# Performance work log

Measured on AMD Instinct MI355X. Metric: run time of the kernel, lower is better.

## Reference

```python
import jax, jax.numpy as jnp
import numpy as np
from jax import lax

C = 256
HEADS = 8
H2 = HEADS // 2          # heads per branch
HD = C // HEADS          # head dim = 32
SR = 4                   # spatial reduction ratio
WS = 7                   # window size (hard-coded in source)
SCALE = HD ** -0.5
EPS = 1e-5


def _window_partition(t, H, W, D):
    # t: [B, h, N, c] -> [B*h*nW, WS^3, c]
    B, h, N, c = t.shape
    t = t.reshape(B * h, H // WS, WS, W // WS, WS, D // WS, WS, c)
    t = t.transpose(0, 1, 3, 5, 2, 4, 6, 7)
    return t.reshape(-1, WS * WS * WS, c)


def _window_reverse(w, H, W, D, head):
    # w: [BH*nW, WS^3, c] -> [B, N, head*c] (heads interleaved into channels)
    nW = (H // WS) * (W // WS) * (D // WS)
    BH = w.shape[0] // nW
    x = w.reshape(BH, H // WS, W // WS, D // WS, WS, WS, WS, -1)
    x = x.transpose(0, 1, 4, 2, 5, 3, 6, 7).reshape(BH, H, W, D, -1)
    B = BH // head
    x = x.reshape(B, head, H, W, D, -1).transpose(0, 2, 3, 4, 1, 5)
    return x.reshape(B, H * W * D, -1)


def setup_inputs() -> dict:
    key = jax.random.key(0)
    ks = jax.random.split(key, 16)
    B, H, W, D = 1, 28, 28, 28
    N = H * W * D
    tn = lambda k, shp: jax.random.normal(k, shp, jnp.float32) * 0.02
    # conv fan-out inits (per source _init_weights)
    lepe_fan = 3 * 3 * C // C  # depthwise: groups=C
    sr_fan = SR * SR * C
    return {
        "x": jax.random.normal(ks[0], (B, N, C), jnp.float32),
        "H": H, "W": W, "D": D,
        "lepe_w": tn(ks[1], (C, C)),
        "lepe_b": jnp.zeros((C,), jnp.float32),
        "lepe_conv_w": jax.random.normal(ks[2], (C, 1, 3, 3, 3), jnp.float32) * np.sqrt(2.0 / lepe_fan),
        "lepe_conv_b": jnp.zeros((C,), jnp.float32),
        "sr_w": jax.random.normal(ks[3], (C, C, SR, SR, SR), jnp.float32) * np.sqrt(2.0 / sr_fan),
        "sr_b": jnp.zeros((C,), jnp.float32),
        "norm_g": jnp.ones((C,), jnp.float32),
        "norm_b": jnp.zeros((C,), jnp.float32),
        "q1_w": tn(ks[4], (C // 2, C)),
        "kv1_w": tn(ks[5], (C, C)),
        "q2_w": tn(ks[6], (C // 2, C)),
        "kv2_w": tn(ks[7], (C, C)),
        "proj_w": tn(ks[8], (C, C)),
        "proj_b": jnp.zeros((C,), jnp.float32),
    }


def _forward(x, lepe_w, lepe_b, lepe_conv_w, lepe_conv_b, sr_w, sr_b,
             norm_g, norm_b, q1_w, kv1_w, q2_w, kv2_w, proj_w, proj_b,
             H, W, D):
    B, N, _ = x.shape
    # --- LePE: linear -> depthwise Conv3d over (H,W,D) ---
    y = x @ lepe_w.T + lepe_b                              # [B,N,C]
    y = y.transpose(0, 2, 1).reshape(B, C, H, W, D)
    lepe = lax.conv_general_dilated(
        y, lepe_conv_w, window_strides=(1, 1, 1), padding='SAME',
        dimension_numbers=('NCDHW', 'OIDHW', 'NCDHW'), feature_group_count=C)
    lepe = (lepe + lepe_conv_b[None, :, None, None, None])
    lepe = lepe.reshape(B, C, N).transpose(0, 2, 1)        # [B,N,C]

    x_ = x.transpose(0, 2, 1).reshape(B, C, H, W, D)

    # --- Branch 1: spatially-reduced global attention (heads 0..3) ---
    q1 = (x @ q1_w.T).reshape(B, N, H2, HD).transpose(0, 2, 1, 3)   # [B,h2,N,hd]
    x1 = lax.conv_general_dilated(
        x_, sr_w, window_strides=(SR, SR, SR), padding='VALID',
        dimension_numbers=('NCDHW', 'OIDHW', 'NCDHW'))
    x1 = x1 + sr_b[None, :, None, None, None]
    x1 = x1.reshape(B, C, -1).transpose(0, 2, 1)                    # [B,Nr,C]
    mu = x1.mean(-1, keepdims=True)
    var = ((x1 - mu) ** 2).mean(-1, keepdims=True)
    x1 = (x1 - mu) * lax.rsqrt(var + EPS) * norm_g + norm_b
    x1 = jax.nn.gelu(x1, approximate=False)
    Nr = x1.shape[1]
    kv1 = (x1 @ kv1_w.T).reshape(B, Nr, 2, H2, HD).transpose(2, 0, 3, 1, 4)
    k1, v1 = kv1[0], kv1[1]                                         # [B,h2,Nr,hd]
    attn1 = jax.nn.softmax(jnp.einsum('bhnd,bhmd->bhnm', q1, k1) * SCALE, axis=-1)
    o1 = jnp.einsum('bhnm,bhmd->bhnd', attn1, v1)
    o1 = o1.transpose(0, 2, 1, 3).reshape(B, N, C // 2)

    # --- Branch 2: windowed local attention (heads 4..7) ---
    q2 = (x @ q2_w.T).reshape(B, N, H2, HD).transpose(0, 2, 1, 3)
    kv2 = (x @ kv2_w.T).reshape(B, N, 2, H2, HD).transpose(2, 0, 3, 1, 4)
    k2, v2 = kv2[0], kv2[1]                                         # [B,h2,N,hd]
    q2w = _window_partition(q2, H, W, D)
    k2w = _window_partition(k2, H, W, D)
    v2w = _window_partition(v2, H, W, D)
    attn2 = jax.nn.softmax(jnp.einsum('wnd,wmd->wnm', q2w, k2w) * SCALE, axis=-1)
    o2 = jnp.einsum('wnm,wmd->wnd', attn2, v2w)
    o2 = _window_reverse(o2, H, W, D, H2)                           # [B,N,C/2]

    out = jnp.concatenate([o1, o2], axis=-1)
    return (out + lepe) @ proj_w.T + proj_b


def reference(x, H, W, D, lepe_w, lepe_b, lepe_conv_w, lepe_conv_b,
              sr_w, sr_b, norm_g, norm_b, q1_w, kv1_w, q2_w, kv2_w,
              proj_w, proj_b):
    return _forward(x, lepe_w, lepe_b, lepe_conv_w, lepe_conv_b, sr_w, sr_b,
                    norm_g, norm_b, q1_w, kv1_w, q2_w, kv2_w, proj_w, proj_b,
                    int(H), int(W), int(D))
```

## Files before the change

kernel.cpp:

```cpp
#include <hip/hip_runtime.h>

#define N_TOK 21952
#define NR    343
#define ATT_SCALE 0.17677669529663687f

typedef unsigned short u16;
typedef short  v8s __attribute__((ext_vector_type(8)));
typedef float  v4f __attribute__((ext_vector_type(4)));

__device__ __forceinline__ float bf2f(unsigned u) {
    return __builtin_bit_cast(float, u << 16);
}
__device__ __forceinline__ u16 f2bf(float f) {
    unsigned u = __builtin_bit_cast(unsigned, f);
    u += 0x7fffu + ((u >> 16) & 1u);
    return (u16)(u >> 16);
}
__device__ __forceinline__ unsigned bfadd2(unsigned a, unsigned b) {
    float lo = bf2f(a & 0xffffu) + bf2f(b & 0xffffu);
    float hi = bf2f(a >> 16)     + bf2f(b >> 16);
    return (unsigned)f2bf(lo) | ((unsigned)f2bf(hi) << 16);
}

__global__ __launch_bounds__(256) void convert_x_kernel(
    const float* __restrict__ x, u16* __restrict__ xb)
{
    size_t i = ((size_t)blockIdx.x * 256 + threadIdx.x) * 8;
    float4 a0 = *(const float4*)(x + i);
    float4 a1 = *(const float4*)(x + i + 4);
    uint4 av;
    av.x = (unsigned)f2bf(a0.x) | ((unsigned)f2bf(a0.y) << 16);
    av.y = (unsigned)f2bf(a0.z) | ((unsigned)f2bf(a0.w) << 16);
    av.z = (unsigned)f2bf(a1.x) | ((unsigned)f2bf(a1.y) << 16);
    av.w = (unsigned)f2bf(a1.z) | ((unsigned)f2bf(a1.w) << 16);
    *(uint4*)(xb + i) = av;
}

#define WSEG0 16384
#define WSEG1 24576
#define WSEG2 32768
#define WSEG3 49152
#define WSEG4 65536
#define WSEG5 81920
#define WSEG6 82112

__global__ __launch_bounds__(256) void convert_w_kernel(
    const float* __restrict__ wl,  const float* __restrict__ wq1,
    const float* __restrict__ wq2, const float* __restrict__ wk2,
    const float* __restrict__ wk1, const float* __restrict__ wp,
    const float* __restrict__ lepe_b,
    u16* wb_comb, u16* wb_k1, u16* wb_p, float* bias_all)
{
    int gid = blockIdx.x * 256 + threadIdx.x;
    if (gid >= WSEG6) return;
    if (gid >= WSEG5) {
        int b = gid - WSEG5;
        float4 v;
        int i = b * 4;
        v.x = (i + 0 < 256) ? lepe_b[i + 0] : 0.f;
        v.y = (i + 1 < 256) ? lepe_b[i + 1] : 0.f;
        v.z = (i + 2 < 256) ? lepe_b[i + 2] : 0.f;
        v.w = (i + 3 < 256) ? lepe_b[i + 3] : 0.f;
        *(float4*)(bias_all + i) = v;
        return;
    }
    const float* s; u16* d; int l; float sc = 1.f;
    if      (gid < WSEG0) { s = wl;  d = wb_comb;           l = gid; }
    else if (gid < WSEG1) { s = wq1; d = wb_comb + 65536;   l = gid - WSEG0; sc = ATT_SCALE; }
    else if (gid < WSEG2) { s = wq2; d = wb_comb + 98304;   l = gid - WSEG1; sc = ATT_SCALE; }
    else if (gid < WSEG3) { s = wk2; d = wb_comb + 131072;  l = gid - WSEG2; }
    else if (gid < WSEG4) { s = wk1; d = wb_k1;             l = gid - WSEG3; }
    else                  { s = wp;  d = wb_p;              l = gid - WSEG4; }
    float4 v = *(const float4*)(s + (size_t)l * 4);
    *(ushort4*)(d + (size_t)l * 4) =
        make_ushort4(f2bf(v.x * sc), f2bf(v.y * sc), f2bf(v.z * sc), f2bf(v.w * sc));
}

__global__ __launch_bounds__(256) void convert_sr_kernel(
    const float* __restrict__ wsr, u16* __restrict__ wt)
{
    int u  = blockIdx.x * 256 + threadIdx.x;
    int co = u >> 8, ci = u & 255;
    const float* src = wsr + (size_t)co * 16384 + ci * 64;
#pragma unroll
    for (int t4 = 0; t4 < 16; t4++) {
        float4 v = *(const float4*)(src + t4 * 4);
        int t = t4 * 4;
        wt[(size_t)(t + 0) * 65536 + co * 256 + ci] = f2bf(v.x);
        wt[(size_t)(t + 1) * 65536 + co * 256 + ci] = f2bf(v.y);
        wt[(size_t)(t + 2) * 65536 + co * 256 + ci] = f2bf(v.z);
        wt[(size_t)(t + 3) * 65536 + co * 256 + ci] = f2bf(v.w);
    }
}

#define LDK 136

__global__ __launch_bounds__(256, 3) void gemm_k256(
    const u16* __restrict__ A, const u16* __restrict__ A2,
    const u16* __restrict__ W, const float* __restrict__ bias,
    void* __restrict__ outp, int M, int ldout, int mode, int nwg, int NT)
{
    __shared__ u16 Asm[128 * LDK];
    __shared__ u16 Bsm[64 * LDK];
    const int tid = threadIdx.x;

    int bid = blockIdx.x;
    int q = nwg >> 3, r = nwg & 7;
    int xcd = bid & 7, idx = bid >> 3;
    int wgid = (xcd < r ? xcd * (q + 1) : r * (q + 1) + (xcd - r) * q) + idx;
    const int m0 = (wgid / NT) * 128;
    const int n0 = (wgid % NT) * 64;

    const int wave = tid >> 6, lane = tid & 63;
    const int wm = (wave & 1) * 64, wn = (wave >> 1) * 32;
    const int fr = lane & 15, fq = lane >> 4;

    v4f acc[4][2];
#pragma unroll
    for (int i = 0; i < 4; i++)
#pragma unroll
        for (int j = 0; j < 2; j++) acc[i][j] = (v4f){0.f, 0.f, 0.f, 0.f};

    for (int ph = 0; ph < 2; ph++) {
        const int kb = ph * 128;
#pragma unroll
        for (int i = 0; i < 8; i++) {
            int u = tid + i * 256;
            int rr = u >> 4, seg = (u & 15) * 8;
            uint4 av = make_uint4(0, 0, 0, 0);
            int m = m0 + rr;
            if (m < M) {
                av = *(const uint4*)(A + (size_t)m * 256 + kb + seg);
                if (A2) {
                    uint4 bv = *(const uint4*)(A2 + (size_t)m * 256 + kb + seg);
                    av.x = bfadd2(av.x, bv.x); av.y = bfadd2(av.y, bv.y);
                    av.z = bfadd2(av.z, bv.z); av.w = bfadd2(av.w, bv.w);
                }
            }
            *(uint4*)(Asm + rr * LDK + seg) = av;
        }
#pragma unroll
        for (int i = 0; i < 4; i++) {
            int u = tid + i * 256;
            int rr = u >> 4, seg = (u & 15) * 8;
            uint4 wv = *(const uint4*)(W + (size_t)(n0 + rr) * 256 + kb + seg);
            *(uint4*)(Bsm + rr * LDK + seg) = wv;
        }
        __syncthreads();

#pragma unroll
        for (int kk = 0; kk < 128; kk += 32) {
            v8s af[4], bf[2];
#pragma unroll
            for (int i = 0; i < 4; i++)
                af[i] = *(const v8s*)(Asm + (wm + i * 16 + fr) * LDK + kk + fq * 8);
#pragma unroll
            for (int j = 0; j < 2; j++)
                bf[j] = *(const v8s*)(Bsm + (wn + j * 16 + fr) * LDK + kk + fq * 8);
#pragma unroll
            for (int i = 0; i < 4; i++)
#pragma unroll
                for (int j = 0; j < 2; j++)
                    acc[i][j] = __builtin_amdgcn_mfma_f32_16x16x32_bf16(
                        af[i], bf[j], acc[i][j], 0, 0, 0);
        }
        __syncthreads();
    }

    float* outf = (float*)outp;
    u16*   outb = (u16*)outp;
#pragma unroll
    for (int i = 0; i < 4; i++) {
#pragma unroll
        for (int j = 0; j < 2; j++) {
            int col = n0 + wn + j * 16 + fr;
#pragma unroll
            for (int rr = 0; rr < 4; rr++) {
                int row = m0 + wm + i * 16 + fq * 4 + rr;
                if (row >= M) continue;
                float v = acc[i][j][rr];
                if (bias) v += bias[col];
                if (mode == 0) outb[(size_t)row * ldout + col] = f2bf(v);
                else           outf[(size_t)row * ldout + col] = v;
            }
        }
    }
}

#define LDA 40

__global__ __launch_bounds__(256) void sr_gemm(
    const u16* __restrict__ xb, const u16* __restrict__ Wt,
    float* __restrict__ partials)
{
    __shared__ u16 Asm[128 * LDA];
    __shared__ u16 Bsm[64 * LDA];
    const int tid = threadIdx.x;
    const int m0 = blockIdx.x * 128;
    const int n0 = blockIdx.y * 64;
    const int z  = blockIdx.z;
    const int wave = tid >> 6, lane = tid & 63;
    const int wm = (wave & 1) * 64, wn = (wave >> 1) * 32;
    const int fr = lane & 15, fq = lane >> 4;

    v4f acc[4][2];
#pragma unroll
    for (int i = 0; i < 4; i++)
#pragma unroll
        for (int j = 0; j < 2; j++) acc[i][j] = (v4f){0.f, 0.f, 0.f, 0.f};

    for (int it = 0; it < 16; it++) {
        int tap = z * 2 + (it >> 3);
        int ci0 = (it & 7) * 32;
        int kz = tap >> 4, ky = (tap >> 2) & 3, kx = tap & 3;
#pragma unroll
        for (int i = 0; i < 2; i++) {
            int u = tid + i * 256;
            int r = u >> 2, seg = (u & 3) * 8;
            uint4 av = make_uint4(0, 0, 0, 0);
            int p = m0 + r;
            if (p < NR) {
                int pz = p / 49, pr = p % 49, py = pr / 7, px = pr % 7;
                int n = (pz * 4 + kz) * 784 + (py * 4 + ky) * 28 + (px * 4 + kx);
                av = *(const uint4*)(xb + (size_t)n * 256 + ci0 + seg);
            }
            *(uint4*)(Asm + r * LDA + seg) = av;
        }
        {
            int r = tid >> 2, seg = (tid & 3) * 8;
            uint4 wv = *(const uint4*)(Wt + (size_t)tap * 65536 +
                                       (size_t)(n0 + r) * 256 + ci0 + seg);
            *(uint4*)(Bsm + r * LDA + seg) = wv;
        }
        __syncthreads();

        v8s af[4], bfr[2];
#pragma unroll
        for (int i = 0; i < 4; i++)
            af[i] = *(const v8s*)(Asm + (wm + i * 16 + fr) * LDA + fq * 8);
#pragma unroll
        for (int j = 0; j < 2; j++)
            bfr[j] = *(const v8s*)(Bsm + (wn + j * 16 + fr) * LDA + fq * 8);
#pragma unroll
        for (int i = 0; i < 4; i++)
#pragma unroll
            for (int j = 0; j < 2; j++)
                acc[i][j] = __builtin_amdgcn_mfma_f32_16x16x32_bf16(
                    af[i], bfr[j], acc[i][j], 0, 0, 0);
        __syncthreads();
    }

    float* dst = partials + (size_t)z * (NR * 256);
#pragma unroll
    for (int i = 0; i < 4; i++) {
#pragma unroll
        for (int j = 0; j < 2; j++) {
            int col = n0 + wn + j * 16 + fr;
#pragma unroll
            for (int r = 0; r < 4; r++) {
                int row = m0 + wm + i * 16 + fq * 4 + r;
                if (row < NR) dst[(size_t)row * 256 + col] = acc[i][j][r];
            }
        }
    }
}

__global__ __launch_bounds__(256) void ln_gelu_kernel(
    const float* __restrict__ partials, const float* __restrict__ srb,
    const float* __restrict__ g, const float* __restrict__ b,
    u16* __restrict__ out)
{
    int row = blockIdx.x, c = threadIdx.x;
    float v = srb[c];
#pragma unroll
    for (int s = 0; s < 32; s++)
        v += partials[(size_t)s * (NR * 256) + row * 256 + c];
    float s1 = v, s2 = v * v;
#pragma unroll
    for (int off = 1; off < 64; off <<= 1) {
        s1 += __shfl_xor(s1, off);
        s2 += __shfl_xor(s2, off);
    }
    __shared__ float ws[4], ws2[4];
    int wave = c >> 6, lane = c & 63;
    if (lane == 0) { ws[wave] = s1; ws2[wave] = s2; }
    __syncthreads();
    float mean = (ws[0] + ws[1] + ws[2] + ws[3]) * (1.f / 256.f);
    float m2   = (ws2[0] + ws2[1] + ws2[2] + ws2[3]) * (1.f / 256.f);
    float var  = m2 - mean * mean;
    float xn = (v - mean) * rsqrtf(var + 1e-5f) * g[c] + b[c];
    out[row * 256 + c] = f2bf(0.5f * xn * (1.f + erff(xn * 0.70710678118654752f)));
}

__global__ __launch_bounds__(256) void dwconv_kernel(
    const u16* __restrict__ xall, const float* __restrict__ w,
    const float* __restrict__ bias, u16* __restrict__ out)
{
    __shared__ float sm[216 * 64];
    __shared__ float sw[64 * 27];
    const int tid = threadIdx.x;
    const int t  = blockIdx.x;
    const int g  = blockIdx.y;
    const int tz = t / 49, tr = t % 49, ty = tr / 7, tx = tr % 7;

    for (int u = tid; u < 64 * 27; u += 256) sw[u] = w[g * 64 * 27 + u];

    for (int u = tid; u < 216 * 8; u += 256) {
        int r = u >> 3, c8 = (u & 7) * 8;
        int vz = tz * 4 - 1 + r / 36;
        int rem = r % 36;
        int vy = ty * 4 - 1 + rem / 6;
        int vx = tx * 4 - 1 + rem % 6;
        float f[8];
        if ((unsigned)vz < 28u && (unsigned)vy < 28u && (unsigned)vx < 28u) {
            int n = vz * 784 + vy * 28 + vx;
            uint4 raw = *(const uint4*)(xall + (size_t)n * 768 + g * 64 + c8);
            f[0] = bf2f(raw.x & 0xffffu); f[1] = bf2f(raw.x >> 16);
            f[2] = bf2f(raw.y & 0xffffu); f[3] = bf2f(raw.y >> 16);
            f[4] = bf2f(raw.z & 0xffffu); f[5] = bf2f(raw.z >> 16);
            f[6] = bf2f(raw.w & 0xffffu); f[7] = bf2f(raw.w >> 16);
        } else {
#pragma unroll
            for (int i = 0; i < 8; i++) f[i] = 0.f;
        }
        float* dst = &sm[r * 64 + c8];
        *(float4*)dst       = make_float4(f[0], f[1], f[2], f[3]);
        *(float4*)(dst + 4) = make_float4(f[4], f[5], f[6], f[7]);
    }
    __syncthreads();

    const int c  = tid & 63;
    const int ch = g * 64 + c;
    float wreg[27];
#pragma unroll
    for (int j = 0; j < 27; j++) wreg[j] = sw[c * 27 + j];
    const float bc = bias[ch];

    const int vbase = (tid >> 6) * 16;
    for (int v = vbase; v < vbase + 16; v++) {
        int vz = v >> 4, vy = (v >> 2) & 3, vx = v & 3;
        float a = bc;
#pragma unroll
        for (int dz = 0; dz < 3; dz++)
#pragma unroll
            for (int dy = 0; dy < 3; dy++)
#pragma unroll
                for (int dx = 0; dx < 3; dx++)
                    a = fmaf(sm[((vz + dz) * 36 + (vy + dy) * 6 + (vx + dx)) * 64 + c],
                             wreg[dz * 9 + dy * 3 + dx], a);
        int n = (tz * 4 + vz) * 784 + (ty * 4 + vy) * 28 + (tx * 4 + vx);
        out[(size_t)n * 256 + ch] = f2bf(a);
    }
}

#define KP  40
#define VTP 360
#define PP  40

__global__ __launch_bounds__(256) void attn1_kernel(
    const u16* __restrict__ xall, const u16* __restrict__ kv1,
    u16* __restrict__ o)
{
    __shared__ u16 Ks[352 * KP];
    __shared__ u16 VTs[32 * VTP];
    __shared__ u16 Ps[4 * 16 * PP];
    const int tid = threadIdx.x;
    const int h = blockIdx.y;
    const int qbase = blockIdx.x * 352;
    const int mt0 = blockIdx.z * 11;
    const int wave = tid >> 6, lane = tid & 63;
    const int fr = lane & 15, fq = lane >> 4;

    for (int u = tid; u < 352 * 4; u += 256) {
        int r = u >> 2, seg = u & 3;
        uint4 kq = make_uint4(0, 0, 0, 0), vq = make_uint4(0, 0, 0, 0);
        if (r < NR) {
            kq = *(const uint4*)(kv1 + (size_t)r * 256 + h * 32 + seg * 8);
            vq = *(const uint4*)(kv1 + (size_t)r * 256 + 128 + h * 32 + seg * 8);
        }
        *(uint4*)(Ks + r * KP + seg * 8) = kq;
        int d0 = seg * 8;
        VTs[(d0 + 0) * VTP + r] = (u16)(vq.x & 0xffffu);
        VTs[(d0 + 1) * VTP + r] = (u16)(vq.x >> 16);
        VTs[(d0 + 2) * VTP + r] = (u16)(vq.y & 0xffffu);
        VTs[(d0 + 3) * VTP + r] = (u16)(vq.y >> 16);
        VTs[(d0 + 4) * VTP + r] = (u16)(vq.z & 0xffffu);
        VTs[(d0 + 5) * VTP + r] = (u16)(vq.z >> 16);
        VTs[(d0 + 6) * VTP + r] = (u16)(vq.w & 0xffffu);
        VTs[(d0 + 7) * VTP + r] = (u16)(vq.w >> 16);
    }
    __syncthreads();

    u16* Pw = Ps + wave * 16 * PP;
    for (int mt = mt0 + wave; mt < mt0 + 11; mt += 4) {
        int qrow = qbase + mt * 16 + fr;
        v8s aq = {0, 0, 0, 0, 0, 0, 0, 0};
        if (qrow < N_TOK)
            aq = *(const v8s*)(xall + (size_t)qrow * 768 + 256 + h * 32 + fq * 8);

        v4f s[22];
#pragma unroll
        for (int t = 0; t < 22; t++) {
            v8s bk = *(const v8s*)(Ks + (t * 16 + fr) * KP + fq * 8);
            s[t] = __builtin_amdgcn_mfma_f32_16x16x32_bf16(
                aq, bk, (v4f){0.f, 0.f, 0.f, 0.f}, 0, 0, 0);
        }
        if (fr >= 7) {
#pragma unroll
            for (int r = 0; r < 4; r++) s[21][r] = -1e30f;
        }

        float inv_l[4];
#pragma unroll
        for (int r = 0; r < 4; r++) {
            float m = s[0][r];
#pragma unroll
            for (int t = 1; t < 22; t++) m = fmaxf(m, s[t][r]);
#pragma unroll
            for (int off = 1; off < 16; off <<= 1) m = fmaxf(m, __shfl_xor(m, off));
            float l = 0.f;
#pragma unroll
            for (int t = 0; t < 22; t++) {
                v4f sv = s[t];
                float p = __expf(sv[r] - m);
                sv[r] = p; s[t] = sv;
                l += p;
            }
#pragma unroll
            for (int off = 1; off < 16; off <<= 1) l += __shfl_xor(l, off);
            inv_l[r] = 1.f / l;
        }

        v4f o0 = {0.f, 0.f, 0.f, 0.f}, o1 = {0.f, 0.f, 0.f, 0.f};
#pragma unroll
        for (int kt = 0; kt < 11; kt++) {
#pragma unroll
            for (int tt = 0; tt < 2; tt++) {
                int t = kt * 2 + tt;
#pragma unroll
                for (int r = 0; r < 4; r++)
                    Pw[(fq * 4 + r) * PP + tt * 16 + fr] = f2bf(s[t][r]);
            }
            __asm__ volatile("s_waitcnt lgkmcnt(0)" ::: "memory");
            v8s ap  = *(const v8s*)(Pw + fr * PP + fq * 8);
            v8s bv0 = *(const v8s*)(VTs + fr * VTP + kt * 32 + fq * 8);
            v8s bv1 = *(const v8s*)(VTs + (16 + fr) * VTP + kt * 32 + fq * 8);
            o0 = __builtin_amdgcn_mfma_f32_16x16x32_bf16(ap, bv0, o0, 0, 0, 0);
            o1 = __builtin_amdgcn_mfma_f32_16x16x32_bf16(ap, bv1, o1, 0, 0, 0);
        }

#pragma unroll
        for (int r = 0; r < 4; r++) {
            int n = qbase + mt * 16 + fq * 4 + r;
            if (n < N_TOK) {
                u16* op = o + (size_t)n * 256 + h * 32;
                op[fr]      = f2bf(o0[r] * inv_l[r]);
                op[16 + fr] = f2bf(o1[r] * inv_l[r]);
            }
        }
    }
}

__global__ __launch_bounds__(256) void attn2_kernel(
    const u16* __restrict__ xall, u16* __restrict__ o)
{
    __shared__ u16 Ks[352 * KP];
    __shared__ u16 VTs[32 * VTP];
    __shared__ u16 Ps[4 * 16 * PP];
    const int tid = threadIdx.x;
    const int h  = blockIdx.y;
    const int wi = blockIdx.x;
    const int zb = (wi >> 4) & 3, yb = (wi >> 2) & 3, xb = wi & 3;
    const int mt0 = blockIdx.z * 11;
    const int wave = tid >> 6, lane = tid & 63;
    const int fr = lane & 15, fq = lane >> 4;

    for (int u = tid; u < 352 * 4; u += 256) {
        int r = u >> 2, seg = u & 3;
        uint4 kq = make_uint4(0, 0, 0, 0), vq = make_uint4(0, 0, 0, 0);
        if (r < NR) {
            int mz = r / 49, mr = r % 49, my = mr / 7, mx = mr % 7;
            int nk = (zb * 7 + mz) * 784 + (yb * 7 + my) * 28 + (xb * 7 + mx);
            const u16* base = xall + (size_t)nk * 768 + 512;
            kq = *(const uint4*)(base + h * 32 + seg * 8);
            vq = *(const uint4*)(base + 128 + h * 32 + seg * 8);
        }
        *(uint4*)(Ks + r * KP + seg * 8) = kq;
        int d0 = seg * 8;
        VTs[(d0 + 0) * VTP + r] = (u16)(vq.x & 0xffffu);
        VTs[(d0 + 1) * VTP + r] = (u16)(vq.x >> 16);
        VTs[(d0 + 2) * VTP + r] = (u16)(vq.y & 0xffffu);
        VTs[(d0 + 3) * VTP + r] = (u16)(vq.y >> 16);
        VTs[(d0 + 4) * VTP + r] = (u16)(vq.z & 0xffffu);
        VTs[(d0 + 5) * VTP + r] = (u16)(vq.z >> 16);
        VTs[(d0 + 6) * VTP + r] = (u16)(vq.w & 0xffffu);
        VTs[(d0 + 7) * VTP + r] = (u16)(vq.w >> 16);
    }
    __syncthreads();

    u16* Pw = Ps + wave * 16 * PP;
    for (int mt = mt0 + wave; mt < mt0 + 11; mt += 4) {
        int tw = mt * 16 + fr;
        v8s aq = {0, 0, 0, 0, 0, 0, 0, 0};
        if (tw < NR) {
            int wz = tw / 49, tr2 = tw % 49, wy = tr2 / 7, wx = tr2 % 7;
            int nq = (zb * 7 + wz) * 784 + (yb * 7 + wy) * 28 + (xb * 7 + wx);
            aq = *(const v8s*)(xall + (size_t)nq * 768 + 384 + h * 32 + fq * 8);
        }

        v4f s[22];
#pragma unroll
        for (int t = 0; t < 22; t++) {
            v8s bk = *(const v8s*)(Ks + (t * 16 + fr) * KP + fq * 8);
            s[t] = __builtin_amdgcn_mfma_f32_16x16x32_bf16(
                aq, bk, (v4f){0.f, 0.f, 0.f, 0.f}, 0, 0, 0);
        }
        if (fr >= 7) {
#pragma unroll
            for (int r = 0; r < 4; r++) s[21][r] = -1e30f;
        }

        float inv_l[4];
#pragma unroll
        for (int r = 0; r < 4; r++) {
            float m = s[0][r];
#pragma unroll
            for (int t = 1; t < 22; t++) m = fmaxf(m, s[t][r]);
#pragma unroll
            for (int off = 1; off < 16; off <<= 1) m = fmaxf(m, __shfl_xor(m, off));
            float l = 0.f;
#pragma unroll
            for (int t = 0; t < 22; t++) {
                v4f sv = s[t];
                float p = __expf(sv[r] - m);
                sv[r] = p; s[t] = sv;
                l += p;
            }
#pragma unroll
            for (int off = 1; off < 16; off <<= 1) l += __shfl_xor(l, off);
            inv_l[r] = 1.f / l;
        }

        v4f o0 = {0.f, 0.f, 0.f, 0.f}, o1 = {0.f, 0.f, 0.f, 0.f};
#pragma unroll
        for (int kt = 0; kt < 11; kt++) {
#pragma unroll
            for (int tt = 0; tt < 2; tt++) {
                int t = kt * 2 + tt;
#pragma unroll
                for (int r = 0; r < 4; r++)
                    Pw[(fq * 4 + r) * PP + tt * 16 + fr] = f2bf(s[t][r]);
            }
            __asm__ volatile("s_waitcnt lgkmcnt(0)" ::: "memory");
            v8s ap  = *(const v8s*)(Pw + fr * PP + fq * 8);
            v8s bv0 = *(const v8s*)(VTs + fr * VTP + kt * 32 + fq * 8);
            v8s bv1 = *(const v8s*)(VTs + (16 + fr) * VTP + kt * 32 + fq * 8);
            o0 = __builtin_amdgcn_mfma_f32_16x16x32_bf16(ap, bv0, o0, 0, 0, 0);
            o1 = __builtin_amdgcn_mfma_f32_16x16x32_bf16(ap, bv1, o1, 0, 0, 0);
        }

#pragma unroll
        for (int r = 0; r < 4; r++) {
            int ts = mt * 16 + fq * 4 + r;
            if (ts < NR) {
                int wz = ts / 49, tr2 = ts % 49, wy = tr2 / 7, wx = tr2 % 7;
                int nq = (zb * 7 + wz) * 784 + (yb * 7 + wy) * 28 + (xb * 7 + wx);
                u16* op = o + (size_t)nq * 256 + 128 + h * 32;
                op[fr]      = f2bf(o0[r] * inv_l[r]);
                op[16 + fr] = f2bf(o1[r] * inv_l[r]);
            }
        }
    }
}

extern "C" void kernel_launch(void* const* d_in, const int* in_sizes, int n_in,
                              void* d_out, int out_size, void* d_ws, size_t ws_size,
                              hipStream_t stream)
{
    const float* x       = (const float*)d_in[0];
    const float* lepe_w  = (const float*)d_in[4];
    const float* lepe_b  = (const float*)d_in[5];
    const float* lconv_w = (const float*)d_in[6];
    const float* lconv_b = (const float*)d_in[7];
    const float* sr_w    = (const float*)d_in[8];
    const float* sr_b    = (const float*)d_in[9];
    const float* norm_g  = (const float*)d_in[10];
    const float* norm_b  = (const float*)d_in[11];
    const float* q1_w    = (const float*)d_in[12];
    const float* kv1_w   = (const float*)d_in[13];
    const float* q2_w    = (const float*)d_in[14];
    const float* kv2_w   = (const float*)d_in[15];
    const float* proj_w  = (const float*)d_in[16];
    const float* proj_b  = (const float*)d_in[17];
    float* out = (float*)d_out;

    const size_t NC = (size_t)N_TOK * 256;

    float* partials = (float*)d_ws;
    float* bias_all = partials + 32 * (NR * 256);
    u16* xb     = (u16*)(bias_all + 768);
    u16* xall   = xb + NC;
    u16* lepeb  = xall + (size_t)N_TOK * 768;
    u16* colb   = lepeb + NC;
    u16* x1b    = colb + NC;
    u16* kv1b   = x1b + NR * 256;
    u16* wb_comb = kv1b + NR * 256;
    u16* wb_k1  = wb_comb + 196608;
    u16* wb_p   = wb_k1 + 65536;
    u16* wsr_t  = wb_p + 65536;
    size_t need = (size_t)(32 * NR * 256 + 768) * 4 +
                  (NC + (size_t)N_TOK * 768 + 3 * NC + 2 * (size_t)NR * 256 +
                   196608 + 2 * 65536 + 4194304) * 2;
    if (ws_size < need) return;

    convert_w_kernel<<<dim3(321), 256, 0, stream>>>(
        lepe_w, q1_w, q2_w, kv2_w, kv1_w, proj_w, lepe_b,
        wb_comb, wb_k1, wb_p, bias_all);
    convert_sr_kernel<<<dim3(256), 256, 0, stream>>>(sr_w, wsr_t);
    convert_x_kernel<<<dim3(2744), 256, 0, stream>>>(x, xb);
    gemm_k256<<<dim3(172 * 12), 256, 0, stream>>>(
        xb, nullptr, wb_comb, bias_all, xall, N_TOK, 768, 0, 172 * 12, 12);
    dwconv_kernel<<<dim3(343, 4), 256, 0, stream>>>(xall, lconv_w, lconv_b, lepeb);
    sr_gemm<<<dim3(3, 4, 32), 256, 0, stream>>>(xb, wsr_t, partials);
    ln_gelu_kernel<<<dim3(NR), 256, 0, stream>>>(partials, sr_b, norm_g, norm_b, x1b);
    gemm_k256<<<dim3(3 * 4), 256, 0, stream>>>(
        x1b, nullptr, wb_k1, nullptr, kv1b, NR, 256, 0, 3 * 4, 4);
    attn1_kernel<<<dim3(63, 4, 2), 256, 0, stream>>>(xall, kv1b, colb);
    attn2_kernel<<<dim3(64, 4, 2), 256, 0, stream>>>(xall, colb);
    gemm_k256<<<dim3(172 * 4), 256, 0, stream>>>(
        colb, lepeb, wb_p, proj_b, out, N_TOK, 256, 1, 172 * 4, 4);
}
```

Baseline: 284.7 us.

## Double-buffer K-tiles in the K=256 GEMM with register prefetch

The K=256 GEMM is rewritten to walk K in eight 32-wide steps. Each step uses double-buffered LDS tiles, and the next tile's global loads are issued into registers before the current tile's MFMAs run. The LDS footprint shrinks from two 128-wide-K tiles to two 32-wide-K buffers, and launch bounds are raised to allow 4 workgroups per CU. In exchange it needs eight barriers instead of four and more live registers for the prefetched data.

```diff
diff --git a/kernel.cpp b/kernel.cpp
--- a/kernel.cpp
+++ b/kernel.cpp
@@ -93,21 +93,21 @@
     }
 }
 
-#define LDK 136
-
-__global__ __launch_bounds__(256, 3) void gemm_k256(
+#define LDA 40
+
+__global__ __launch_bounds__(256, 4) void gemm_pipe(
     const u16* __restrict__ A, const u16* __restrict__ A2,
     const u16* __restrict__ W, const float* __restrict__ bias,
     void* __restrict__ outp, int M, int ldout, int mode, int nwg, int NT)
 {
-    __shared__ u16 Asm[128 * LDK];
-    __shared__ u16 Bsm[64 * LDK];
+    __shared__ u16 Asm[2][128 * LDA];
+    __shared__ u16 Bsm[2][64 * LDA];
     const int tid = threadIdx.x;
 
     int bid = blockIdx.x;
-    int q = nwg >> 3, r = nwg & 7;
+    int q = nwg >> 3, r8 = nwg & 7;
     int xcd = bid & 7, idx = bid >> 3;
-    int wgid = (xcd < r ? xcd * (q + 1) : r * (q + 1) + (xcd - r) * q) + idx;
+    int wgid = (xcd < r8 ? xcd * (q + 1) : r8 * (q + 1) + (xcd - r8) * q) + idx;
     const int m0 = (wgid / NT) * 128;
     const int n0 = (wgid % NT) * 64;
 
@@ -115,48 +115,64 @@
     const int wm = (wave & 1) * 64, wn = (wave >> 1) * 32;
     const int fr = lane & 15, fq = lane >> 4;
 
+    const int ar0 = tid >> 2;
+    const int ar1 = ar0 + 64;
+    const int seg = (tid & 3) * 8;
+    const bool g0 = (m0 + ar0) < M;
+    const bool g1 = (m0 + ar1) < M;
+    const u16* pA0 = A + (size_t)(m0 + ar0) * 256 + seg;
+    const u16* pA1 = A + (size_t)(m0 + ar1) * 256 + seg;
+    const u16* pB  = W + (size_t)(n0 + ar0) * 256 + seg;
+    const u16* pC0 = A2 + (size_t)(m0 + ar0) * 256 + seg;
+    const u16* pC1 = A2 + (size_t)(m0 + ar1) * 256 + seg;
+
+    uint4 ra0, ra1, rb, rc0, rc1;
+    const bool has2 = (A2 != nullptr);
+
+    auto LOAD = [&](int ph) {
+        int kk = ph * 32;
+        ra0 = g0 ? *(const uint4*)(pA0 + kk) : make_uint4(0, 0, 0, 0);
+        ra1 = g1 ? *(const uint4*)(pA1 + kk) : make_uint4(0, 0, 0, 0);
+        rb  = *(const uint4*)(pB + kk);
+        if (has2) {
+            rc0 = g0 ? *(const uint4*)(pC0 + kk) : make_uint4(0, 0, 0, 0);
+            rc1 = g1 ? *(const uint4*)(pC1 + kk) : make_uint4(0, 0, 0, 0);
+        }
+    };
+    auto WRITE = [&](int buf) {
+        uint4 a0 = ra0, a1 = ra1;
+        if (has2) {
+            a0.x = bfadd2(a0.x, rc0.x); a0.y = bfadd2(a0.y, rc0.y);
+            a0.z = bfadd2(a0.z, rc0.z); a0.w = bfadd2(a0.w, rc0.w);
+            a1.x = bfadd2(a1.x, rc1.x); a1.y = bfadd2(a1.y, rc1.y);
+            a1.z = bfadd2(a1.z, rc1.z); a1.w = bfadd2(a1.w, rc1.w);
+        }
+        *(uint4*)(Asm[buf] + ar0 * LDA + seg) = a0;
+        *(uint4*)(Asm[buf] + ar1 * LDA + seg) = a1;
+        *(uint4*)(Bsm[buf] + ar0 * LDA + seg) = rb;
+    };
+
     v4f acc[4][2];
 #pragma unroll
     for (int i = 0; i < 4; i++)
 #pragma unroll
         for (int j = 0; j < 2; j++) acc[i][j] = (v4f){0.f, 0.f, 0.f, 0.f};
 
-    for (int ph = 0; ph < 2; ph++) {
-        const int kb = ph * 128;
-#pragma unroll
-        for (int i = 0; i < 8; i++) {
-            int u = tid + i * 256;
-            int rr = u >> 4, seg = (u & 15) * 8;
-            uint4 av = make_uint4(0, 0, 0, 0);
-            int m = m0 + rr;
-            if (m < M) {
-                av = *(const uint4*)(A + (size_t)m * 256 + kb + seg);
-                if (A2) {
-                    uint4 bv = *(const uint4*)(A2 + (size_t)m * 256 + kb + seg);
-                    av.x = bfadd2(av.x, bv.x); av.y = bfadd2(av.y, bv.y);
-                    av.z = bfadd2(av.z, bv.z); av.w = bfadd2(av.w, bv.w);
-                }
-            }
-            *(uint4*)(Asm + rr * LDK + seg) = av;
-        }
-#pragma unroll
-        for (int i = 0; i < 4; i++) {
-            int u = tid + i * 256;
-            int rr = u >> 4, seg = (u & 15) * 8;
-            uint4 wv = *(const uint4*)(W + (size_t)(n0 + rr) * 256 + kb + seg);
-            *(uint4*)(Bsm + rr * LDK + seg) = wv;
-        }
-        __syncthreads();
-
-#pragma unroll
-        for (int kk = 0; kk < 128; kk += 32) {
+    LOAD(0);
+    WRITE(0);
+    __syncthreads();
+
+    int cur = 0;
+    for (int ph = 0; ph < 8; ph++) {
+        if (ph + 1 < 8) LOAD(ph + 1);
+        {
             v8s af[4], bf[2];
 #pragma unroll
             for (int i = 0; i < 4; i++)
-                af[i] = *(const v8s*)(Asm + (wm + i * 16 + fr) * LDK + kk + fq * 8);
+                af[i] = *(const v8s*)(Asm[cur] + (wm + i * 16 + fr) * LDA + fq * 8);
 #pragma unroll
             for (int j = 0; j < 2; j++)
-                bf[j] = *(const v8s*)(Bsm + (wn + j * 16 + fr) * LDK + kk + fq * 8);
+                bf[j] = *(const v8s*)(Bsm[cur] + (wn + j * 16 + fr) * LDA + fq * 8);
 #pragma unroll
             for (int i = 0; i < 4; i++)
 #pragma unroll
@@ -164,7 +180,9 @@
                     acc[i][j] = __builtin_amdgcn_mfma_f32_16x16x32_bf16(
                         af[i], bf[j], acc[i][j], 0, 0, 0);
         }
+        if (ph + 1 < 8) WRITE(cur ^ 1);
         __syncthreads();
+        cur ^= 1;
     }
 
     float* outf = (float*)outp;
@@ -186,8 +204,6 @@
         }
     }
 }
-
-#define LDA 40
 
 __global__ __launch_bounds__(256) void sr_gemm(
     const u16* __restrict__ xb, const u16* __restrict__ Wt,
@@ -618,15 +634,15 @@
         wb_comb, wb_k1, wb_p, bias_all);
     convert_sr_kernel<<<dim3(256), 256, 0, stream>>>(sr_w, wsr_t);
     convert_x_kernel<<<dim3(2744), 256, 0, stream>>>(x, xb);
-    gemm_k256<<<dim3(172 * 12), 256, 0, stream>>>(
+    gemm_pipe<<<dim3(172 * 12), 256, 0, stream>>>(
         xb, nullptr, wb_comb, bias_all, xall, N_TOK, 768, 0, 172 * 12, 12);
     dwconv_kernel<<<dim3(343, 4), 256, 0, stream>>>(xall, lconv_w, lconv_b, lepeb);
     sr_gemm<<<dim3(3, 4, 32), 256, 0, stream>>>(xb, wsr_t, partials);
     ln_gelu_kernel<<<dim3(NR), 256, 0, stream>>>(partials, sr_b, norm_g, norm_b, x1b);
-    gemm_k256<<<dim3(3 * 4), 256, 0, stream>>>(
+    gemm_pipe<<<dim3(3 * 4), 256, 0, stream>>>(
         x1b, nullptr, wb_k1, nullptr, kv1b, NR, 256, 0, 3 * 4, 4);
     attn1_kernel<<<dim3(63, 4, 2), 256, 0, stream>>>(xall, kv1b, colb);
     attn2_kernel<<<dim3(64, 4, 2), 256, 0, stream>>>(xall, colb);
-    gemm_k256<<<dim3(172 * 4), 256, 0, stream>>>(
+    gemm_pipe<<<dim3(172 * 4), 256, 0, stream>>>(
         colb, lepeb, wb_p, proj_b, out, N_TOK, 256, 1, 172 * 4, 4);
 }
```

After: 272.7 us. 4.2% less time.
